# Optimization experiments

Hardware: AMD Instinct MI355X
Metric: run time of the kernel (lower is better)

The kernel has to match this reference:

```python
import jax, jax.numpy as jnp
import numpy as np

MARGIN = 0.1

def setup_inputs() -> dict:
    key = jax.random.key(0)
    k1, k2 = jax.random.split(key)
    embeddings = jax.random.normal(k1, (8192, 128), dtype=jnp.float32)
    labels = jax.random.randint(k2, (8192,), 0, 64, dtype=jnp.int64)
    return {"embeddings": embeddings, "labels": labels}

def reference(embeddings, labels):
    # sim[i,j] = <e_i, e_j>
    sim = embeddings @ embeddings.T  # [n, n]
    eq = labels[:, None] == labels[None, :]  # pos mask (includes diagonal)
    # per entry: exp(margin - sim) for positives, exp(sim - margin) for negatives
    terms = jnp.where(eq, jnp.exp(MARGIN - sim), jnp.exp(sim - MARGIN))
    # loss_i = log(sum_j terms[i,j]); loss = mean_i loss_i
    return jnp.mean(jnp.log(jnp.sum(terms, axis=1)))
```

## Files before the change

### kernel.cpp

```cpp
#include <hip/hip_runtime.h>
#include <hip/hip_bf16.h>

#define N 8192
#define D 128
#define LOG2E  1.44269504088896f
#define LN2    0.69314718055995f

typedef __attribute__((ext_vector_type(8))) short bf16x8;
typedef __attribute__((ext_vector_type(4))) float f32x4;

#if __has_builtin(__builtin_amdgcn_exp2f)
#define EXP2(x) __builtin_amdgcn_exp2f(x)
#else
#define EXP2(x) exp2f(x)
#endif
#if __has_builtin(__builtin_amdgcn_logf)
#define LOG2(x) __builtin_amdgcn_logf(x)
#else
#define LOG2(x) log2f(x)
#endif

typedef const __attribute__((address_space(1))) unsigned int as1_u32c;
typedef __attribute__((address_space(3))) unsigned int as3_u32;

static __device__ __forceinline__ unsigned short f2bf(float f) {
    union { float f; unsigned int u; } x;
    x.f = f;
    unsigned int r = ((x.u >> 16) & 1u) + 0x7FFFu;
    return (unsigned short)((x.u + r) >> 16);
}

__global__ void prep_kernel(const float* __restrict__ E,
                            uint4* __restrict__ Eb2,
                            float* __restrict__ rowsum) {
    const int j = blockIdx.x * 256 + threadIdx.x;
    const int l  = j & 15;
    const int q  = (j >> 4) & 3;
    const int kk = (j >> 6) & 3;
    const int S  = j >> 8;
    const float4* src = (const float4*)(E + (size_t)(S * 16 + l) * D + kk * 32 + q * 8);
    float4 f0 = src[0], f1 = src[1];
    uint4 o;
    o.x = f2bf(f0.x) | ((unsigned)f2bf(f0.y) << 16);
    o.y = f2bf(f0.z) | ((unsigned)f2bf(f0.w) << 16);
    o.z = f2bf(f1.x) | ((unsigned)f2bf(f1.y) << 16);
    o.w = f2bf(f1.z) | ((unsigned)f2bf(f1.w) << 16);
    Eb2[j] = o;
    if (j < N) rowsum[j] = 0.0f;
}

__global__ __launch_bounds__(256) void fused_kernel(
        const unsigned short* __restrict__ Eb2,
        const int* __restrict__ labels,
        float* __restrict__ rowsum) {
    __shared__ uint4 btile4[2048];
    __shared__ int   labC[128];
    __shared__ int   labR[128];
    __shared__ float colacc[128];

    const int tid  = threadIdx.x;
    const int wid  = tid >> 6;
    const int lane = tid & 63;
    const int q = lane >> 4;
    const int l = lane & 15;

    const int b = blockIdx.x;
    int r = (int)(64.5f - sqrtf(64.5f * 64.5f - 2.0f * (float)b));
    while ((r + 1) * 64 - ((r + 1) * r) / 2 <= b) ++r;
    while (r * 64 - (r * (r - 1)) / 2 > b) --r;
    const int c = r + (b - (r * 64 - (r * (r - 1)) / 2));
    const bool diag = (r == c);
    const int tile_m0 = r * 128;
    const int n_begin = c * 128;
    const int mrow0 = wid * 32;

    const char* base = (const char*)Eb2;
    char* bt = (char*)btile4;

    bf16x8 a[2][4];
#pragma unroll
    for (int g = 0; g < 2; ++g) {
        const char* pa = base + (size_t)(r * 8 + wid * 2 + g) * 4096 + lane * 16;
#pragma unroll
        for (int kk = 0; kk < 4; ++kk)
            a[g][kk] = *(const bf16x8*)(pa + kk * 1024);
    }

    {
        const char* gB = base + (size_t)(c * 8) * 4096;
#pragma unroll
        for (int u = 0; u < 8; ++u) {
            const int m = wid * 8 + u;
            __builtin_amdgcn_global_load_lds(
                (as1_u32c*)(gB + m * 1024 + lane * 16),
                (as3_u32*)(bt + m * 1024),
                16, 0, 0);
        }
    }

    if (tid < 128) { labC[tid] = labels[n_begin + tid]; colacc[tid] = 0.0f; }
    else           { labR[tid - 128] = labels[tile_m0 + (tid - 128)]; }
    asm volatile("s_waitcnt vmcnt(0)" ::: "memory");
    __syncthreads();

    int lrow[8];
#pragma unroll
    for (int g = 0; g < 2; ++g)
#pragma unroll
        for (int rr = 0; rr < 4; ++rr)
            lrow[g * 4 + rr] = labR[mrow0 + g * 16 + q * 4 + rr];

    float sum[8];
#pragma unroll
    for (int i = 0; i < 8; ++i) sum[i] = 0.0f;

#pragma clang loop unroll(disable)
    for (int s = 0; s < 8; ++s) {
        const char* pb = bt + s * 4096 + lane * 16;
        bf16x8 b0 = *(const bf16x8*)(pb);
        bf16x8 b1 = *(const bf16x8*)(pb + 1024);
        bf16x8 b2 = *(const bf16x8*)(pb + 2048);
        bf16x8 b3 = *(const bf16x8*)(pb + 3072);
        const int lc = labC[s * 16 + l];

        f32x4 acc0 = (f32x4){0.f, 0.f, 0.f, 0.f};
        f32x4 acc1 = (f32x4){0.f, 0.f, 0.f, 0.f};
        acc0 = __builtin_amdgcn_mfma_f32_16x16x32_bf16(a[0][0], b0, acc0, 0, 0, 0);
        acc0 = __builtin_amdgcn_mfma_f32_16x16x32_bf16(a[0][1], b1, acc0, 0, 0, 0);
        acc0 = __builtin_amdgcn_mfma_f32_16x16x32_bf16(a[0][2], b2, acc0, 0, 0, 0);
        acc0 = __builtin_amdgcn_mfma_f32_16x16x32_bf16(a[0][3], b3, acc0, 0, 0, 0);
        acc1 = __builtin_amdgcn_mfma_f32_16x16x32_bf16(a[1][0], b0, acc1, 0, 0, 0);
        acc1 = __builtin_amdgcn_mfma_f32_16x16x32_bf16(a[1][1], b1, acc1, 0, 0, 0);
        acc1 = __builtin_amdgcn_mfma_f32_16x16x32_bf16(a[1][2], b2, acc1, 0, 0, 0);
        acc1 = __builtin_amdgcn_mfma_f32_16x16x32_bf16(a[1][3], b3, acc1, 0, 0, 0);

        float cp = 0.0f;
#pragma unroll
        for (int g = 0; g < 2; ++g) {
#pragma unroll
            for (int rr = 0; rr < 4; ++rr) {
                float sv = (g == 0) ? acc0[rr] : acc1[rr];
                bool eq = (lrow[g * 4 + rr] == lc);
                float cc = eq ? -LOG2E : LOG2E;
                float term = EXP2(cc * (sv - 0.1f));
                sum[g * 4 + rr] += term;
                cp += term;
            }
        }
        if (!diag) {
            cp += __shfl_xor(cp, 16);
            cp += __shfl_xor(cp, 32);
            if (q == 0) atomicAdd(&colacc[s * 16 + l], cp);
        }
    }

#pragma unroll
    for (int i = 0; i < 8; ++i) {
        float v = sum[i];
        v += __shfl_xor(v, 1);
        v += __shfl_xor(v, 2);
        v += __shfl_xor(v, 4);
        v += __shfl_xor(v, 8);
        sum[i] = v;
    }
    if (l == 0) {
#pragma unroll
        for (int g = 0; g < 2; ++g)
#pragma unroll
            for (int rr = 0; rr < 4; ++rr)
                atomicAdd(&rowsum[tile_m0 + mrow0 + g * 16 + q * 4 + rr],
                          sum[g * 4 + rr]);
    }

    __syncthreads();
    if (!diag && tid < 128)
        atomicAdd(&rowsum[n_begin + tid], colacc[tid]);
}

__global__ void finalize_kernel(const float* __restrict__ rowsum,
                                float* __restrict__ out) {
    __shared__ float red[4];
    const int tid = threadIdx.x;
    float v = 0.0f;
#pragma unroll 8
    for (int k = 0; k < 32; ++k) v += LOG2(rowsum[tid + 256 * k]);
    v *= LN2;
#pragma unroll
    for (int off = 1; off <= 32; off <<= 1) v += __shfl_xor(v, off);
    if ((tid & 63) == 0) red[tid >> 6] = v;
    __syncthreads();
    if (tid == 0)
        out[0] = (red[0] + red[1] + red[2] + red[3]) * (1.0f / (float)N);
}

extern "C" void kernel_launch(void* const* d_in, const int* in_sizes, int n_in,
                              void* d_out, int out_size, void* d_ws, size_t ws_size,
                              hipStream_t stream) {
    const float* E = (const float*)d_in[0];
    const int* labels = (const int*)d_in[1];
    float* out = (float*)d_out;

    unsigned short* Eb2 = (unsigned short*)d_ws;
    float* rowsum = (float*)((char*)d_ws + (size_t)N * D * 2);

    prep_kernel<<<512, 256, 0, stream>>>(E, (uint4*)Eb2, rowsum);
    fused_kernel<<<2080, 256, 0, stream>>>(Eb2, labels, rowsum);
    finalize_kernel<<<1, 256, 0, stream>>>(rowsum, out);
}
```

Measured before the change: 86.72 us.

## Fuse finalize into main kernel via last-block counter and read B directly from global

```diff
diff --git a/kernel.cpp b/kernel.cpp
--- a/kernel.cpp
+++ b/kernel.cpp
@@ -20,9 +20,6 @@
 #define LOG2(x) log2f(x)
 #endif
 
-typedef const __attribute__((address_space(1))) unsigned int as1_u32c;
-typedef __attribute__((address_space(3))) unsigned int as3_u32;
-
 static __device__ __forceinline__ unsigned short f2bf(float f) {
     union { float f; unsigned int u; } x;
     x.f = f;
@@ -32,7 +29,8 @@
 
 __global__ void prep_kernel(const float* __restrict__ E,
                             uint4* __restrict__ Eb2,
-                            float* __restrict__ rowsum) {
+                            float* __restrict__ rowsum,
+                            unsigned int* __restrict__ counter) {
     const int j = blockIdx.x * 256 + threadIdx.x;
     const int l  = j & 15;
     const int q  = (j >> 4) & 3;
@@ -47,16 +45,20 @@
     o.w = f2bf(f1.z) | ((unsigned)f2bf(f1.w) << 16);
     Eb2[j] = o;
     if (j < N) rowsum[j] = 0.0f;
+    if (j == 0) *counter = 0u;
 }
 
 __global__ __launch_bounds__(256) void fused_kernel(
         const unsigned short* __restrict__ Eb2,
         const int* __restrict__ labels,
-        float* __restrict__ rowsum) {
-    __shared__ uint4 btile4[2048];
+        float* __restrict__ rowsum,
+        unsigned int* __restrict__ counter,
+        float* __restrict__ out) {
     __shared__ int   labC[128];
     __shared__ int   labR[128];
     __shared__ float colacc[128];
+    __shared__ float red[4];
+    __shared__ unsigned int tk;
 
     const int tid  = threadIdx.x;
     const int wid  = tid >> 6;
@@ -75,7 +77,6 @@
     const int mrow0 = wid * 32;
 
     const char* base = (const char*)Eb2;
-    char* bt = (char*)btile4;
 
     bf16x8 a[2][4];
 #pragma unroll
@@ -86,21 +87,8 @@
             a[g][kk] = *(const bf16x8*)(pa + kk * 1024);
     }
 
-    {
-        const char* gB = base + (size_t)(c * 8) * 4096;
-#pragma unroll
-        for (int u = 0; u < 8; ++u) {
-            const int m = wid * 8 + u;
-            __builtin_amdgcn_global_load_lds(
-                (as1_u32c*)(gB + m * 1024 + lane * 16),
-                (as3_u32*)(bt + m * 1024),
-                16, 0, 0);
-        }
-    }
-
     if (tid < 128) { labC[tid] = labels[n_begin + tid]; colacc[tid] = 0.0f; }
     else           { labR[tid - 128] = labels[tile_m0 + (tid - 128)]; }
-    asm volatile("s_waitcnt vmcnt(0)" ::: "memory");
     __syncthreads();
 
     int lrow[8];
@@ -116,7 +104,7 @@
 
 #pragma clang loop unroll(disable)
     for (int s = 0; s < 8; ++s) {
-        const char* pb = bt + s * 4096 + lane * 16;
+        const char* pb = base + (size_t)(c * 8 + s) * 4096 + lane * 16;
         bf16x8 b0 = *(const bf16x8*)(pb);
         bf16x8 b1 = *(const bf16x8*)(pb + 1024);
         bf16x8 b2 = *(const bf16x8*)(pb + 2048);
@@ -175,22 +163,29 @@
     __syncthreads();
     if (!diag && tid < 128)
         atomicAdd(&rowsum[n_begin + tid], colacc[tid]);
-}
-
-__global__ void finalize_kernel(const float* __restrict__ rowsum,
-                                float* __restrict__ out) {
-    __shared__ float red[4];
-    const int tid = threadIdx.x;
-    float v = 0.0f;
+
+    __threadfence();
+    __syncthreads();
+    if (tid == 0) tk = atomicAdd(counter, 1u);
+    __syncthreads();
+    if (tk == 2079u) {
+        __threadfence();
+        float v = 0.0f;
 #pragma unroll 8
-    for (int k = 0; k < 32; ++k) v += LOG2(rowsum[tid + 256 * k]);
-    v *= LN2;
-#pragma unroll
-    for (int off = 1; off <= 32; off <<= 1) v += __shfl_xor(v, off);
-    if ((tid & 63) == 0) red[tid >> 6] = v;
-    __syncthreads();
-    if (tid == 0)
-        out[0] = (red[0] + red[1] + red[2] + red[3]) * (1.0f / (float)N);
+        for (int k = 0; k < 32; ++k) {
+            float s = __hip_atomic_load(&rowsum[tid + 256 * k],
+                                        __ATOMIC_RELAXED,
+                                        __HIP_MEMORY_SCOPE_AGENT);
+            v += LOG2(s);
+        }
+        v *= LN2;
+#pragma unroll
+        for (int off = 1; off <= 32; off <<= 1) v += __shfl_xor(v, off);
+        if ((tid & 63) == 0) red[tid >> 6] = v;
+        __syncthreads();
+        if (tid == 0)
+            out[0] = (red[0] + red[1] + red[2] + red[3]) * (1.0f / (float)N);
+    }
 }
 
 extern "C" void kernel_launch(void* const* d_in, const int* in_sizes, int n_in,
@@ -202,8 +197,8 @@
 
     unsigned short* Eb2 = (unsigned short*)d_ws;
     float* rowsum = (float*)((char*)d_ws + (size_t)N * D * 2);
-
-    prep_kernel<<<512, 256, 0, stream>>>(E, (uint4*)Eb2, rowsum);
-    fused_kernel<<<2080, 256, 0, stream>>>(Eb2, labels, rowsum);
-    finalize_kernel<<<1, 256, 0, stream>>>(rowsum, out);
-}
+    unsigned int* counter = (unsigned int*)(rowsum + N);
+
+    prep_kernel<<<512, 256, 0, stream>>>(E, (uint4*)Eb2, rowsum, counter);
+    fused_kernel<<<2080, 256, 0, stream>>>(Eb2, labels, rowsum, counter, out);
+}
```

Result: slower. 203.9 us (+135.1%).
